# Optimization experiments

Measured on AMD Instinct MI355X. Metric: run time of the kernel, lower is better.

The kernel has to match this reference:

```python
import jax, jax.numpy as jnp
import numpy as np
import math

C_IN, L, D, H, DFF = 16, 1024, 128, 8, 512
B = 16
EPS = 1e-5


def layer_norm(x, g, b):
    mu = jnp.mean(x, axis=-1, keepdims=True)
    var = jnp.var(x, axis=-1, keepdims=True)
    return (x - mu) * jax.lax.rsqrt(var + EPS) * g + b


def tape_pe():
    pos = jnp.arange(L, dtype=jnp.float32)[:, None]
    div = jnp.exp(jnp.arange(0, D, 2, dtype=jnp.float32) * (-math.log(10000.0) / D))
    ang = pos * div * (D / L)  # [L, D/2]
    return jnp.stack([jnp.sin(ang), jnp.cos(ang)], axis=-1).reshape(L, D)


def setup_inputs() -> dict:
    key = jax.random.key(0)
    ks = jax.random.split(key, 16)
    d4 = 4 * D
    inp = {
        "x": jax.random.normal(ks[0], (B, C_IN, L), dtype=jnp.float32),
        "conv1_w": jax.random.normal(ks[1], (d4, 1, 1, 7), dtype=jnp.float32) * 0.2,
        "conv1_b": jnp.zeros((d4,), jnp.float32),
        "bn1_g": jnp.ones((d4,), jnp.float32),
        "bn1_b": jnp.zeros((d4,), jnp.float32),
        "conv2_w": jax.random.normal(ks[2], (D, d4, C_IN, 1), dtype=jnp.float32) * (1.0 / math.sqrt(d4 * C_IN)),
        "conv2_b": jnp.zeros((D,), jnp.float32),
        "bn2_g": jnp.ones((D,), jnp.float32),
        "bn2_b": jnp.zeros((D,), jnp.float32),
        "wq": jax.random.normal(ks[3], (D, D), dtype=jnp.float32) / math.sqrt(D),
        "wk": jax.random.normal(ks[4], (D, D), dtype=jnp.float32) / math.sqrt(D),
        "wv": jax.random.normal(ks[5], (D, D), dtype=jnp.float32) / math.sqrt(D),
        "rel_table": jax.random.normal(ks[6], (2 * L - 1, H), dtype=jnp.float32) * 0.02,
        "ln_att_g": jnp.ones((D,), jnp.float32),
        "ln_att_b": jnp.zeros((D,), jnp.float32),
        "ln1_g": jnp.ones((D,), jnp.float32),
        "ln1_b": jnp.zeros((D,), jnp.float32),
        "ln2_g": jnp.ones((D,), jnp.float32),
        "ln2_b": jnp.zeros((D,), jnp.float32),
        "ff_w1": jax.random.normal(ks[7], (DFF, D), dtype=jnp.float32) / math.sqrt(D),
        "ff_b1": jnp.zeros((DFF,), jnp.float32),
        "ff_w2": jax.random.normal(ks[8], (D, DFF), dtype=jnp.float32) / math.sqrt(DFF),
        "ff_b2": jnp.zeros((D,), jnp.float32),
    }
    return inp


def reference(x, conv1_w, conv1_b, bn1_g, bn1_b, conv2_w, conv2_b, bn2_g, bn2_b,
              wq, wk, wv, rel_table, ln_att_g, ln_att_b, ln1_g, ln1_b,
              ln2_g, ln2_b, ff_w1, ff_b1, ff_w2, ff_b2):
    dn = ("NCHW", "OIHW", "NCHW")
    h = x[:, None, :, :]  # [B,1,C_IN,L]
    h = jax.lax.conv_general_dilated(h, conv1_w, (1, 1), ((0, 0), (3, 3)), dimension_numbers=dn)
    h = h + conv1_b[None, :, None, None]
    # BatchNorm2d in eval with running_mean=0, running_var=1
    h = h * (bn1_g * (1.0 / math.sqrt(1.0 + EPS)))[None, :, None, None] + bn1_b[None, :, None, None]
    h = jax.nn.gelu(h, approximate=False)
    h = jax.lax.conv_general_dilated(h, conv2_w, (1, 1), ((0, 0), (0, 0)), dimension_numbers=dn)
    h = h + conv2_b[None, :, None, None]
    h = h * (bn2_g * (1.0 / math.sqrt(1.0 + EPS)))[None, :, None, None] + bn2_b[None, :, None, None]
    h = jax.nn.gelu(h, approximate=False)
    x_src = jnp.transpose(h[:, :, 0, :], (0, 2, 1))  # [B,L,D]

    x_pos = x_src + tape_pe()  # tAPE (dropout is identity in eval)

    dh = D // H
    scale = D ** (-0.5)  # note: full d_model, as in the source
    q = (x_pos @ wq.T).reshape(B, L, H, dh).transpose(0, 2, 1, 3)
    k = (x_pos @ wk.T).reshape(B, L, H, dh).transpose(0, 2, 1, 3)
    v = (x_pos @ wv.T).reshape(B, L, H, dh).transpose(0, 2, 1, 3)
    scores = jnp.einsum("bhqd,bhkd->bhqk", q, k) * scale
    attn = jax.nn.softmax(scores, axis=-1)
    # gathered relative-position bias added AFTER softmax (faithful to source)
    idx = jnp.arange(L)[:, None] - jnp.arange(L)[None, :] + (L - 1)  # [L,L]
    rel_bias = rel_table[idx]  # [L,L,H]
    attn = attn + jnp.transpose(rel_bias, (2, 0, 1))[None]
    out = jnp.einsum("bhqk,bhkd->bhqd", attn, v).transpose(0, 2, 1, 3).reshape(B, L, D)
    out = layer_norm(out, ln_att_g, ln_att_b)  # Attention_Rel_Scl.to_out

    att = layer_norm(x_src + out, ln1_g, ln1_b)
    ff = jax.nn.relu(att @ ff_w1.T + ff_b1) @ ff_w2.T + ff_b2
    y = layer_norm(att + ff, ln2_g, ln2_b)
    return jnp.transpose(y, (0, 2, 1))  # [B,D,L]
```

## Files before the change

kernel.cpp:

```cpp
#include <hip/hip_runtime.h>
#include <math.h>

#define BB   16
#define CIN  16
#define LL   1024
#define DD   128
#define NHH  8
#define DHH  16
#define DF   512

#define INVS 0.9999950000374998f
#define QSCALE 0.08838834764831845f

typedef __attribute__((ext_vector_type(4))) float f32x4;
typedef __attribute__((ext_vector_type(8))) __bf16 bf16x8;

__device__ __forceinline__ float gelu_t(float v) {
    float u = v * v;
    float a = v * fmaf(-0.07135481627f, u, -1.5957691216f);
    float e = __expf(a);
    return v * __builtin_amdgcn_rcpf(1.0f + e);
}

__device__ __forceinline__ unsigned pkbf(float a, float b) {
    union { __bf16 h[2]; unsigned u; } z;
    z.h[0] = (__bf16)a; z.h[1] = (__bf16)b;
    return z.u;
}

#define SWZ(l) ((((l) & 7) ^ (((l) >> 2) & 6)))

__global__ __launch_bounds__(256) void k_prep(
    const float* __restrict__ c2w,
    const float* __restrict__ wq, const float* __restrict__ wk,
    const float* __restrict__ wv,
    const float* __restrict__ w1f, const float* __restrict__ w2f,
    const float* __restrict__ c1w, const float* __restrict__ c1b,
    const float* __restrict__ g1,  const float* __restrict__ bb1,
    __bf16* __restrict__ w2bf,  __bf16* __restrict__ wallbf,
    __bf16* __restrict__ w1fbf, __bf16* __restrict__ w2fbf,
    float* __restrict__ peb, float* __restrict__ w1A, float* __restrict__ b1A)
{
    const int bid = blockIdx.x;
    const int t = threadIdx.x;
    if (bid < 1024) {
        int i = (bid * 256 + t) * 4;
        float4 v = *(const float4*)&c2w[i];
        union { __bf16 h[4]; float2 f2; } u;
        u.h[0] = (__bf16)v.x; u.h[1] = (__bf16)v.y;
        u.h[2] = (__bf16)v.z; u.h[3] = (__bf16)v.w;
        *(float2*)&w2bf[i] = u.f2;
    } else if (bid < 1072) {
        int e = ((bid - 1024) * 256 + t) * 4;
        int sel = e >> 14, r = e & 16383;
        const float* src = (sel == 0) ? wq : ((sel == 1) ? wk : wv);
        float sc = (sel == 0) ? QSCALE : 1.0f;
        float4 v = *(const float4*)&src[r];
        union { __bf16 h[4]; float2 f2; } u;
        u.h[0] = (__bf16)(v.x * sc); u.h[1] = (__bf16)(v.y * sc);
        u.h[2] = (__bf16)(v.z * sc); u.h[3] = (__bf16)(v.w * sc);
        *(float2*)&wallbf[e] = u.f2;
    } else if (bid < 1136) {
        int e = ((bid - 1072) * 256 + t) * 4;
        float4 v = *(const float4*)&w1f[e];
        union { __bf16 h[4]; float2 f2; } u;
        u.h[0] = (__bf16)v.x; u.h[1] = (__bf16)v.y;
        u.h[2] = (__bf16)v.z; u.h[3] = (__bf16)v.w;
        *(float2*)&w1fbf[e] = u.f2;
    } else if (bid < 1200) {
        int e = ((bid - 1136) * 256 + t) * 4;
        float4 v = *(const float4*)&w2f[e];
        union { __bf16 h[4]; float2 f2; } u;
        u.h[0] = (__bf16)v.x; u.h[1] = (__bf16)v.y;
        u.h[2] = (__bf16)v.z; u.h[3] = (__bf16)v.w;
        *(float2*)&w2fbf[e] = u.f2;
    } else if (bid < 1456) {
        int p = (bid - 1200) * 256 + t;
        int l = p >> 6, jj = p & 63;
        float ang = (float)l * expf(-0.14391156831212787f * (float)jj) * 0.125f;
        peb[l * 128 + jj * 2]     = sinf(ang);
        peb[l * 128 + jj * 2 + 1] = cosf(ang);
    } else {
        for (int o = t; o < DF; o += 256) {
            float A = g1[o] * INVS;
            #pragma unroll
            for (int tp = 0; tp < 7; tp++) w1A[o * 8 + tp] = c1w[o * 7 + tp] * A;
            w1A[o * 8 + 7] = 0.0f;
            b1A[o] = fmaf(c1b[o], A, bb1[o]);
        }
    }
}

__global__ __launch_bounds__(512, 4) void k_conv(
    const float* __restrict__ x,
    const float* __restrict__ w1A, const float* __restrict__ b1A,
    const __bf16* __restrict__ w2bf,
    const float* __restrict__ c2b, const float* __restrict__ g2,
    const float* __restrict__ bb2,
    float* __restrict__ xsrc)
{
    const int lt = blockIdx.x;
    const int b  = blockIdx.y;
    const int t  = threadIdx.x;
    const int l0 = lt * 32;

    __shared__ float xs[CIN][40];
    __shared__ __align__(16) __bf16 Ab[2][32 * 256];

    for (int idx = t; idx < CIN * 38; idx += 512) {
        int c = idx / 38, i = idx % 38;
        int l = l0 - 3 + i;
        xs[c][i] = (l >= 0 && l < LL) ? x[(b * CIN + c) * LL + l] : 0.0f;
    }
    __syncthreads();

    const int lane = t & 63;
    const int wv   = t >> 6;
    const int ogu  = __builtin_amdgcn_readfirstlane(wv);
    const int cp   = lane & 7;
    const int lqi  = lane >> 3;
    const int c0   = cp * 2;
    const int lq   = lqi * 4;

    float xw[2][10];
    #pragma unroll
    for (int j = 0; j < 10; j++) {
        xw[0][j] = xs[c0][lq + j];
        xw[1][j] = xs[c0 + 1][lq + j];
    }

    const int l15 = lane & 15, kg = lane >> 4;

    f32x4 acc[2];
    acc[0] = (f32x4){0.f, 0.f, 0.f, 0.f};
    acc[1] = (f32x4){0.f, 0.f, 0.f, 0.f};

    bf16x8 breg[8];

#define BLOAD(CH) do { \
    _Pragma("unroll") \
    for (int kk = 0; kk < 8; kk++) \
        breg[kk] = *(const bf16x8*)&w2bf[ \
            (size_t)(wv * 16 + l15) * 8192 + (size_t)(CH) * 256 + kk * 32 + kg * 8]; \
} while (0)

#define CONV_CHUNK(BUF, CH) do { \
    _Pragma("unroll") \
    for (int j = 0; j < 2; j++) { \
        int o = (CH) * 16 + ogu * 2 + j; \
        f32x4 wA = *(const f32x4*)&w1A[o * 8]; \
        f32x4 wB = *(const f32x4*)&w1A[o * 8 + 4]; \
        float bias = b1A[o]; \
        int kcol = (ogu * 2 + j) * 16 + c0; \
        _Pragma("unroll") \
        for (int dl = 0; dl < 4; dl++) { \
            float h2[2]; \
            _Pragma("unroll") \
            for (int ci = 0; ci < 2; ci++) { \
                float s = fmaf(xw[ci][dl], wA[0], bias); \
                s = fmaf(xw[ci][dl + 1], wA[1], s); \
                s = fmaf(xw[ci][dl + 2], wA[2], s); \
                s = fmaf(xw[ci][dl + 3], wA[3], s); \
                s = fmaf(xw[ci][dl + 4], wB[0], s); \
                s = fmaf(xw[ci][dl + 5], wB[1], s); \
                s = fmaf(xw[ci][dl + 6], wB[2], s); \
                h2[ci] = gelu_t(s); \
            } \
            int l = lq + dl; \
            *(unsigned*)&Ab[BUF][l * 256 + (kcol ^ (SWZ(l) << 3))] = pkbf(h2[0], h2[1]); \
        } \
    } \
} while (0)

#define MFMA_CHUNK(BUF) do { \
    _Pragma("unroll") \
    for (int kk = 0; kk < 8; kk++) { \
        int kb = kk * 32 + kg * 8; \
        _Pragma("unroll") \
        for (int mf = 0; mf < 2; mf++) { \
            int r = mf * 16 + l15; \
            bf16x8 af = *(const bf16x8*)&Ab[BUF][r * 256 + (kb ^ (SWZ(r) << 3))]; \
            acc[mf] = __builtin_amdgcn_mfma_f32_16x16x32_bf16(af, breg[kk], acc[mf], 0, 0, 0); \
        } \
    } \
} while (0)

    BLOAD(0);
    CONV_CHUNK(0, 0);
    __syncthreads();

    for (int ic = 0; ic < 30; ic += 2) {
        MFMA_CHUNK(0);
        BLOAD(ic + 1);
        CONV_CHUNK(1, ic + 1);
        __syncthreads();

        MFMA_CHUNK(1);
        BLOAD(ic + 2);
        CONV_CHUNK(0, ic + 2);
        __syncthreads();
    }
    MFMA_CHUNK(0);
    BLOAD(31);
    CONV_CHUNK(1, 31);
    __syncthreads();
    MFMA_CHUNK(1);

    {
        int d = wv * 16 + l15;
        float A2 = g2[d] * INVS;
        float B2 = fmaf(c2b[d], A2, bb2[d]);
        #pragma unroll
        for (int mf = 0; mf < 2; mf++) {
            #pragma unroll
            for (int r = 0; r < 4; r++) {
                int l = l0 + mf * 16 + kg * 4 + r;
                xsrc[((size_t)b * LL + l) * DD + d] = gelu_t(fmaf(acc[mf][r], A2, B2));
            }
        }
    }
#undef BLOAD
#undef CONV_CHUNK
#undef MFMA_CHUNK
}

__global__ __launch_bounds__(384) void k_qkv(
    const float* __restrict__ xsrc, const float* __restrict__ peb,
    const __bf16* __restrict__ wallbf,
    __bf16* __restrict__ qo, __bf16* __restrict__ ko, __bf16* __restrict__ vo)
{
    const int lt = blockIdx.x, b = blockIdx.y;
    const int t = threadIdx.x;
    const int l0 = lt * 64;

    __shared__ __align__(16) __bf16 Xp[64 * 128];

    for (int e = t; e < 2048; e += 384) {
        int l = e >> 5, d0 = (e & 31) * 4;
        float4 xv = *(const float4*)&xsrc[((size_t)b * LL + l0 + l) * DD + d0];
        float4 pv = *(const float4*)&peb[(size_t)(l0 + l) * DD + d0];
        union { __bf16 h[4]; float2 f2; } u;
        u.h[0] = (__bf16)(xv.x + pv.x); u.h[1] = (__bf16)(xv.y + pv.y);
        u.h[2] = (__bf16)(xv.z + pv.z); u.h[3] = (__bf16)(xv.w + pv.w);
        *(float2*)&Xp[l * 128 + (d0 ^ (SWZ(l) << 3))] = u.f2;
    }
    __syncthreads();

    const int w = t >> 6, lane = t & 63;
    const int l15 = lane & 15, kg = lane >> 4;
    const int wsel = w >> 1, hb = w & 1;

    bf16x8 breg[16];
    #pragma unroll
    for (int nf = 0; nf < 4; nf++)
        #pragma unroll
        for (int kk = 0; kk < 4; kk++)
            breg[nf * 4 + kk] = *(const bf16x8*)&wallbf[
                (size_t)wsel * 16384 + (size_t)(hb * 64 + nf * 16 + l15) * 128 + kk * 32 + kg * 8];

    f32x4 acc[4][4];
    #pragma unroll
    for (int mf = 0; mf < 4; mf++)
        #pragma unroll
        for (int nf = 0; nf < 4; nf++) acc[mf][nf] = (f32x4){0.f, 0.f, 0.f, 0.f};

    #pragma unroll
    for (int kk = 0; kk < 4; kk++) {
        int kb = kk * 32 + kg * 8;
        bf16x8 af[4];
        #pragma unroll
        for (int mf = 0; mf < 4; mf++) {
            int r = mf * 16 + l15;
            af[mf] = *(const bf16x8*)&Xp[r * 128 + (kb ^ (SWZ(r) << 3))];
        }
        #pragma unroll
        for (int mf = 0; mf < 4; mf++)
            #pragma unroll
            for (int nf = 0; nf < 4; nf++)
                acc[mf][nf] = __builtin_amdgcn_mfma_f32_16x16x32_bf16(
                    af[mf], breg[nf * 4 + kk], acc[mf][nf], 0, 0, 0);
    }

    __bf16* op = (wsel == 0) ? qo : ((wsel == 1) ? ko : vo);
    #pragma unroll
    for (int mf = 0; mf < 4; mf++) {
        #pragma unroll
        for (int nf = 0; nf < 4; nf++) {
            int h = hb * 4 + nf;
            #pragma unroll
            for (int r = 0; r < 4; r++) {
                int l = l0 + mf * 16 + kg * 4 + r;
                op[(((size_t)b * NHH + h) * LL + l) * DHH + l15] = (__bf16)acc[mf][nf][r];
            }
        }
    }
}

__global__ __launch_bounds__(256) void k_attn(
    const __bf16* __restrict__ q, const __bf16* __restrict__ k,
    const __bf16* __restrict__ v, const float* __restrict__ rel,
    float* __restrict__ out)
{
    const int bh = blockIdx.x;
    const int qt = blockIdx.y;
    const int h  = bh & 7;
    const int t  = threadIdx.x;
    const int w  = t >> 6, lane = t & 63;
    const int g  = lane >> 4, qi = lane & 15;
    const int xq = (qi & 7) << 3;
    const int qbase = qt * 128 + w * 32;

    __shared__ __align__(16) __bf16 lds[16384];
    __bf16* Vl = lds;
    __bf16* Pw = lds + 4096 + w * 2048;
    __bf16* R0 = lds + 12288;
    __bf16* R1 = lds + 14336;

    for (int i = t; i < 2048; i += 256) {
        R0[i] = (__bf16)((i <= 2046) ? rel[(size_t)(2046 - i) * NHH + h] : 0.0f);
        R1[i] = (__bf16)((i <= 2045) ? rel[(size_t)(2045 - i) * NHH + h] : 0.0f);
    }

    bf16x8 qf[2];
    {
        union { unsigned u[4]; bf16x8 v8; } uz;
        uz.u[0] = uz.u[1] = uz.u[2] = uz.u[3] = 0u;
        #pragma unroll
        for (int n = 0; n < 2; n++) {
            qf[n] = uz.v8;
            if (g < 2)
                qf[n] = *(const bf16x8*)&q[((size_t)bh * LL + qbase + n * 16 + qi) * DHH + g * 8];
        }
    }

    f32x4 accp[2], accb[2];
    #pragma unroll
    for (int n = 0; n < 2; n++) {
        accp[n] = (f32x4){0.f, 0.f, 0.f, 0.f};
        accb[n] = (f32x4){0.f, 0.f, 0.f, 0.f};
    }
    float mrun[2] = {-INFINITY, -INFINITY};
    float lrun[2] = {0.f, 0.f};

    const f32x4 zero4 = (f32x4){0.f, 0.f, 0.f, 0.f};

#define PROC_N(Sn, n) do { \
    float mx = Sn[0][0]; \
    _Pragma("unroll") \
    for (int f = 0; f < 8; f++) { \
        _Pragma("unroll") \
        for (int r = 0; r < 4; r++) if (f || r) mx = fmaxf(mx, Sn[f][r]); } \
    mx = fmaxf(mx, __shfl_xor(mx, 16, 64)); \
    mx = fmaxf(mx, __shfl_xor(mx, 32, 64)); \
    float mnew = fmaxf(mrun[n], mx); \
    float sf = __expf(mrun[n] - mnew); \
    mrun[n] = mnew; \
    lrun[n] *= sf; \
    accp[n][0] *= sf; accp[n][1] *= sf; accp[n][2] *= sf; accp[n][3] *= sf; \
    float ls = 0.f; \
    _Pragma("unroll") \
    for (int f = 0; f < 8; f++) { \
        float p0 = __expf(Sn[f][0] - mnew), p1 = __expf(Sn[f][1] - mnew); \
        float p2 = __expf(Sn[f][2] - mnew), p3 = __expf(Sn[f][3] - mnew); \
        ls += (p0 + p1) + (p2 + p3); \
        unsigned* pp = (unsigned*)(Pw + (qi * 128 + ((f * 16 + g * 4) ^ xq))); \
        pp[0] = pkbf(p0, p1); pp[1] = pkbf(p2, p3); \
    } \
    ls += __shfl_xor(ls, 16, 64); ls += __shfl_xor(ls, 32, 64); \
    lrun[n] += ls; \
    int qoff = 1023 - (qbase + (n) * 16 + qi) + k0; \
    _Pragma("unroll") \
    for (int c = 0; c < 4; c++) { \
        bf16x8 vf = *(const bf16x8*)&Vbuf[qi * 128 + ((c * 32 + g * 8) ^ xq)]; \
        bf16x8 pf = *(const bf16x8*)&Pw[qi * 128 + ((c * 32 + g * 8) ^ xq)]; \
        int idx = qoff + c * 32 + 8 * g; \
        const unsigned* tb = (const unsigned*)((idx & 1) ? R1 : R0); \
        unsigned s_ = (unsigned)idx >> 1; \
        union { unsigned u[4]; bf16x8 v8; } bu; \
        bu.u[0] = tb[s_]; bu.u[1] = tb[s_ + 1]; \
        bu.u[2] = tb[s_ + 2]; bu.u[3] = tb[s_ + 3]; \
        accp[n] = __builtin_amdgcn_mfma_f32_16x16x32_bf16(vf, pf, accp[n], 0, 0, 0); \
        accb[n] = __builtin_amdgcn_mfma_f32_16x16x32_bf16(vf, bu.v8, accb[n], 0, 0, 0); \
    } \
} while (0)

    for (int kt = 0; kt < 8; kt++) {
        const int k0 = kt * 128;
        {
            int kr = t >> 1, d0 = (t & 1) * 8;
            bf16x8 b8 = *(const bf16x8*)&v[((size_t)bh * LL + k0 + kr) * DHH + d0];
            __bf16* dst = Vl + (kt & 1) * 2048;
            #pragma unroll
            for (int i = 0; i < 8; i++) {
                int d = d0 + i;
                dst[d * 128 + (kr ^ ((d & 7) << 3))] = b8[i];
            }
        }
        __syncthreads();
        const __bf16* Vbuf = Vl + (kt & 1) * 2048;

        f32x4 S0[8], S1[8];
        #pragma unroll
        for (int f = 0; f < 8; f++) {
            bf16x8 kf = *(const bf16x8*)&k[((size_t)bh * LL + k0 + f * 16 + qi) * DHH + (g & 1) * 8];
            S0[f] = __builtin_amdgcn_mfma_f32_16x16x32_bf16(kf, qf[0], zero4, 0, 0, 0);
            S1[f] = __builtin_amdgcn_mfma_f32_16x16x32_bf16(kf, qf[1], zero4, 0, 0, 0);
        }

        PROC_N(S0, 0);
        PROC_N(S1, 1);
    }
#undef PROC_N

    #pragma unroll
    for (int n = 0; n < 2; n++) {
        float inv = 1.0f / lrun[n];
        float4 o;
        o.x = accp[n][0] * inv + accb[n][0];
        o.y = accp[n][1] * inv + accb[n][1];
        o.z = accp[n][2] * inv + accb[n][2];
        o.w = accp[n][3] * inv + accb[n][3];
        *(float4*)&out[((size_t)bh * LL + qbase + n * 16 + qi) * DHH + g * 4] = o;
    }
}

__global__ __launch_bounds__(256) void k_ln(
    const float* __restrict__ ao,  const float* __restrict__ xsrc,
    const float* __restrict__ lag, const float* __restrict__ lab,
    const float* __restrict__ l1g, const float* __restrict__ l1b,
    float* __restrict__ att)
{
    const int lt = blockIdx.x, b = blockIdx.y;
    const int t = threadIdx.x;
    const int l0 = lt * 64;
    __shared__ float tile[64][132];

    #pragma unroll
    for (int u = 0; u < 4; u++) {
        int cid = u * 256 + t;
        int hh = cid >> 7, rem = cid & 127;
        int l = rem >> 1, dh0 = (rem & 1) * 8;
        const float* src = &ao[(((size_t)b * NHH + hh) * LL + l0 + l) * DHH + dh0];
        float4 a0 = *(const float4*)src;
        float4 a1 = *(const float4*)(src + 4);
        *(float4*)&tile[l][hh * 16 + dh0]     = a0;
        *(float4*)&tile[l][hh * 16 + dh0 + 4] = a1;
    }
    __syncthreads();

    const int wid = t >> 6, lane = t & 63;
    float2 ga  = *(const float2*)&lag[lane * 2];
    float2 ba  = *(const float2*)&lab[lane * 2];
    float2 g1v = *(const float2*)&l1g[lane * 2];
    float2 b1v = *(const float2*)&l1b[lane * 2];

    for (int rr = 0; rr < 16; rr++) {
        int r = wid * 16 + rr;
        float2 vv = *(const float2*)&tile[r][lane * 2];
        float s = vv.x + vv.y, s2 = vv.x * vv.x + vv.y * vv.y;
        #pragma unroll
        for (int m = 1; m < 64; m <<= 1) { s += __shfl_xor(s, m, 64); s2 += __shfl_xor(s2, m, 64); }
        float mu = s * (1.f / 128.f);
        float var = s2 * (1.f / 128.f) - mu * mu;
        float rs = rsqrtf(var + 1e-5f);
        float o0 = (vv.x - mu) * rs * ga.x + ba.x;
        float o1 = (vv.y - mu) * rs * ga.y + ba.y;
        float2 xv = *(const float2*)&xsrc[((size_t)b * LL + l0 + r) * DD + lane * 2];
        float t0 = xv.x + o0, t1 = xv.y + o1;
        s = t0 + t1; s2 = t0 * t0 + t1 * t1;
        #pragma unroll
        for (int m = 1; m < 64; m <<= 1) { s += __shfl_xor(s, m, 64); s2 += __shfl_xor(s2, m, 64); }
        mu = s * (1.f / 128.f);
        var = s2 * (1.f / 128.f) - mu * mu;
        rs = rsqrtf(var + 1e-5f);
        float a0 = (t0 - mu) * rs * g1v.x + b1v.x;
        float a1 = (t1 - mu) * rs * g1v.y + b1v.y;
        float2 o = {a0, a1};
        *(float2*)&att[((size_t)b * LL + l0 + r) * DD + lane * 2] = o;
    }
}

__global__ __launch_bounds__(512) void k_ff1(
    const float* __restrict__ att, const __bf16* __restrict__ w1fbf,
    const float* __restrict__ b1f, __bf16* __restrict__ ff1b)
{
    const int lt = blockIdx.x, b = blockIdx.y;
    const int t = threadIdx.x;
    const int l0 = lt * 64;

    __shared__ __align__(16) __bf16 Ax[64 * 128];

    #pragma unroll
    for (int it = 0; it < 4; it++) {
        int e = it * 512 + t;
        int l = e >> 5, d0 = (e & 31) * 4;
        float4 xv = *(const float4*)&att[((size_t)b * LL + l0 + l) * DD + d0];
        union { __bf16 h[4]; float2 f2; } u;
        u.h[0] = (__bf16)xv.x; u.h[1] = (__bf16)xv.y;
        u.h[2] = (__bf16)xv.z; u.h[3] = (__bf16)xv.w;
        *(float2*)&Ax[l * 128 + (d0 ^ (SWZ(l) << 3))] = u.f2;
    }
    __syncthreads();

    const int w = t >> 6, lane = t & 63;
    const int l15 = lane & 15, kg = lane >> 4;

    bf16x8 breg[16];
    #pragma unroll
    for (int nf = 0; nf < 4; nf++)
        #pragma unroll
        for (int kk = 0; kk < 4; kk++)
            breg[nf * 4 + kk] = *(const bf16x8*)&w1fbf[
                (size_t)(w * 64 + nf * 16 + l15) * 128 + kk * 32 + kg * 8];

    f32x4 acc[4][4];
    #pragma unroll
    for (int mf = 0; mf < 4; mf++)
        #pragma unroll
        for (int nf = 0; nf < 4; nf++) acc[mf][nf] = (f32x4){0.f, 0.f, 0.f, 0.f};

    #pragma unroll
    for (int kk = 0; kk < 4; kk++) {
        int kb = kk * 32 + kg * 8;
        bf16x8 af[4];
        #pragma unroll
        for (int mf = 0; mf < 4; mf++) {
            int r = mf * 16 + l15;
            af[mf] = *(const bf16x8*)&Ax[r * 128 + (kb ^ (SWZ(r) << 3))];
        }
        #pragma unroll
        for (int mf = 0; mf < 4; mf++)
            #pragma unroll
            for (int nf = 0; nf < 4; nf++)
                acc[mf][nf] = __builtin_amdgcn_mfma_f32_16x16x32_bf16(
                    af[mf], breg[nf * 4 + kk], acc[mf][nf], 0, 0, 0);
    }

    #pragma unroll
    for (int nf = 0; nf < 4; nf++) {
        int n = w * 64 + nf * 16 + l15;
        float bias = b1f[n];
        #pragma unroll
        for (int mf = 0; mf < 4; mf++) {
            #pragma unroll
            for (int r = 0; r < 4; r++) {
                int l = l0 + mf * 16 + kg * 4 + r;
                float vv = fmaxf(acc[mf][nf][r] + bias, 0.0f);
                ff1b[((size_t)b * LL + l) * DF + n] = (__bf16)vv;
            }
        }
    }
}

__global__ __launch_bounds__(512) void k_ff2(
    const __bf16* __restrict__ ff1b, const __bf16* __restrict__ w2fbf,
    const float* __restrict__ b2f, const float* __restrict__ att,
    const float* __restrict__ l2g, const float* __restrict__ l2b,
    float* __restrict__ y)
{
    const int lt = blockIdx.x, b = blockIdx.y;
    const int t = threadIdx.x;
    const int l0 = lt * 64;

    __shared__ __align__(16) __bf16 Ax[64 * 512];
    float* yl = (float*)Ax;

    #pragma unroll
    for (int it = 0; it < 8; it++) {
        int g8 = it * 512 + t;
        int l = g8 >> 6, c8 = g8 & 63;
        bf16x8 v8 = *(const bf16x8*)&ff1b[((size_t)b * LL + l0 + l) * DF + c8 * 8];
        *(bf16x8*)&Ax[l * 512 + ((c8 * 8) ^ (SWZ(l) << 3))] = v8;
    }
    __syncthreads();

    const int w = t >> 6, lane = t & 63;
    const int l15 = lane & 15, kg = lane >> 4;
    const int d = w * 16 + l15;

    bf16x8 breg[16];
    #pragma unroll
    for (int kk = 0; kk < 16; kk++)
        breg[kk] = *(const bf16x8*)&w2fbf[(size_t)d * DF + kk * 32 + kg * 8];

    f32x4 acc[4];
    #pragma unroll
    for (int mf = 0; mf < 4; mf++) acc[mf] = (f32x4){0.f, 0.f, 0.f, 0.f};

    #pragma unroll
    for (int kk = 0; kk < 16; kk++) {
        int kb = kk * 32 + kg * 8;
        #pragma unroll
        for (int mf = 0; mf < 4; mf++) {
            int r = mf * 16 + l15;
            bf16x8 af = *(const bf16x8*)&Ax[r * 512 + (kb ^ (SWZ(r) << 3))];
            acc[mf] = __builtin_amdgcn_mfma_f32_16x16x32_bf16(af, breg[kk], acc[mf], 0, 0, 0);
        }
    }
    __syncthreads();

    {
        float bias = b2f[d];
        #pragma unroll
        for (int mf = 0; mf < 4; mf++) {
            #pragma unroll
            for (int r = 0; r < 4; r++) {
                int l = mf * 16 + kg * 4 + r;
                float res = att[((size_t)b * LL + l0 + l) * DD + d];
                yl[l * 132 + d] = acc[mf][r] + bias + res;
            }
        }
    }
    __syncthreads();

    const int wid = t >> 6;
    float2 gv = *(const float2*)&l2g[lane * 2];
    float2 bv = *(const float2*)&l2b[lane * 2];
    for (int rr = 0; rr < 8; rr++) {
        int r = wid * 8 + rr;
        float2 vv = *(const float2*)&yl[r * 132 + lane * 2];
        float s = vv.x + vv.y, s2 = vv.x * vv.x + vv.y * vv.y;
        #pragma unroll
        for (int m = 1; m < 64; m <<= 1) { s += __shfl_xor(s, m, 64); s2 += __shfl_xor(s2, m, 64); }
        float mu = s * (1.f / 128.f);
        float var = s2 * (1.f / 128.f) - mu * mu;
        float rs = rsqrtf(var + 1e-5f);
        float o0 = (vv.x - mu) * rs * gv.x + bv.x;
        float o1 = (vv.y - mu) * rs * gv.y + bv.y;
        yl[r * 132 + lane * 2]     = o0;
        yl[r * 132 + lane * 2 + 1] = o1;
    }
    __syncthreads();

    {
        int dd = t >> 2, lh = (t & 3) * 16;
        #pragma unroll
        for (int i0 = 0; i0 < 16; i0 += 4) {
            float4 o = { yl[(lh + i0 + 0) * 132 + dd], yl[(lh + i0 + 1) * 132 + dd],
                         yl[(lh + i0 + 2) * 132 + dd], yl[(lh + i0 + 3) * 132 + dd] };
            *(float4*)&y[(size_t)b * DD * LL + (size_t)dd * LL + l0 + lh + i0] = o;
        }
    }
}

extern "C" void kernel_launch(void* const* d_in, const int* in_sizes, int n_in,
                              void* d_out, int out_size, void* d_ws, size_t ws_size,
                              hipStream_t stream)
{
    const float* x   = (const float*)d_in[0];
    const float* c1w = (const float*)d_in[1];
    const float* c1b = (const float*)d_in[2];
    const float* g1  = (const float*)d_in[3];
    const float* bb1 = (const float*)d_in[4];
    const float* c2w = (const float*)d_in[5];
    const float* c2b = (const float*)d_in[6];
    const float* g2  = (const float*)d_in[7];
    const float* bb2 = (const float*)d_in[8];
    const float* wq  = (const float*)d_in[9];
    const float* wk  = (const float*)d_in[10];
    const float* wv  = (const float*)d_in[11];
    const float* rel = (const float*)d_in[12];
    const float* lag = (const float*)d_in[13];
    const float* lab = (const float*)d_in[14];
    const float* l1g = (const float*)d_in[15];
    const float* l1b = (const float*)d_in[16];
    const float* l2g = (const float*)d_in[17];
    const float* l2b = (const float*)d_in[18];
    const float* w1f = (const float*)d_in[19];
    const float* b1f = (const float*)d_in[20];
    const float* w2f = (const float*)d_in[21];
    const float* b2f = (const float*)d_in[22];

    char* W = (char*)d_ws;
    const size_t MB = 1ull << 20;
    float*  xsrc   = (float*)(W);
    float*  abuf   = (float*)(W + 8 * MB);
    float*  attb   = (float*)(W + 16 * MB);
    __bf16* qbuf   = (__bf16*)(W + 24 * MB);
    __bf16* kbuf   = (__bf16*)(W + 28 * MB);
    __bf16* vbuf   = (__bf16*)(W + 32 * MB);
    __bf16* ff1b   = (__bf16*)(W + 36 * MB);
    __bf16* w2bf   = (__bf16*)(W + 52 * MB);
    __bf16* wallbf = (__bf16*)(W + 54 * MB);
    __bf16* w1fbf  = (__bf16*)(W + 54 * MB + 128 * 1024);
    __bf16* w2fbf  = (__bf16*)(W + 54 * MB + 256 * 1024);
    float*  peb    = (float*)(W + 54 * MB + 384 * 1024);
    float*  w1A    = (float*)(W + 54 * MB + 896 * 1024);
    float*  b1A    = (float*)(W + 54 * MB + 912 * 1024);

    k_prep<<<dim3(1457), dim3(256), 0, stream>>>(
        c2w, wq, wk, wv, w1f, w2f, c1w, c1b, g1, bb1,
        w2bf, wallbf, w1fbf, w2fbf, peb, w1A, b1A);
    k_conv<<<dim3(32, 16), dim3(512), 0, stream>>>(x, w1A, b1A, w2bf, c2b, g2, bb2, xsrc);
    k_qkv<<<dim3(16, 16), dim3(384), 0, stream>>>(xsrc, peb, wallbf, qbuf, kbuf, vbuf);
    k_attn<<<dim3(128, 8), dim3(256), 0, stream>>>(qbuf, kbuf, vbuf, rel, abuf);
    k_ln<<<dim3(16, 16), dim3(256), 0, stream>>>(abuf, xsrc, lag, lab, l1g, l1b, attb);
    k_ff1<<<dim3(16, 16), dim3(512), 0, stream>>>(attb, w1fbf, b1f, ff1b);
    k_ff2<<<dim3(16, 16), dim3(512), 0, stream>>>(ff1b, w2fbf, b2f, attb, l2g, l2b, (float*)d_out);
}
```

Before: 240.7 us.

## Retile conv2 waves as 2x4 grid, pack conv1 FMAs and use exp2 GELU

The fused conv kernel's waves are rearranged from eight column strips, each covering all 32 rows, into a 2x4 grid where each wave owns 16 rows by 32 output channels. Each wave now reads half as many shared-memory A fragments but loads twice as many conv2 weight vectors, so total global weight traffic per block doubles. The depthwise conv1 accumulation is rewritten on float2 vectors so the compiler can emit packed FMAs for the two input channels. The tanh-style GELU folds log2(e) into its constants and calls the native exp2 builtin instead of __expf.

New measurement: 350.2 us. +45.5%, slower.

```diff
diff --git a/kernel.cpp b/kernel.cpp
--- a/kernel.cpp
+++ b/kernel.cpp
@@ -12,14 +12,27 @@
 #define INVS 0.9999950000374998f
 #define QSCALE 0.08838834764831845f
 
+typedef __attribute__((ext_vector_type(2))) float f32x2;
 typedef __attribute__((ext_vector_type(4))) float f32x4;
 typedef __attribute__((ext_vector_type(8))) __bf16 bf16x8;
 
 __device__ __forceinline__ float gelu_t(float v) {
     float u = v * v;
-    float a = v * fmaf(-0.07135481627f, u, -1.5957691216f);
-    float e = __expf(a);
+    float a = v * fmaf(-0.10294425f, u, -2.3022082f);
+    float e = __builtin_amdgcn_exp2f(a);
     return v * __builtin_amdgcn_rcpf(1.0f + e);
+}
+
+__device__ __forceinline__ f32x2 gelu2(f32x2 v) {
+    f32x2 u = v * v;
+    f32x2 a = v * (u * (-0.10294425f) + (-2.3022082f));
+    f32x2 e;
+    e.x = __builtin_amdgcn_exp2f(a.x);
+    e.y = __builtin_amdgcn_exp2f(a.y);
+    f32x2 r;
+    r.x = __builtin_amdgcn_rcpf(1.0f + e.x);
+    r.y = __builtin_amdgcn_rcpf(1.0f + e.y);
+    return v * r;
 }
 
 __device__ __forceinline__ unsigned pkbf(float a, float b) {
@@ -115,19 +128,18 @@
     __syncthreads();
 
     const int lane = t & 63;
-    const int wv   = t >> 6;
-    const int ogu  = __builtin_amdgcn_readfirstlane(wv);
+    const int ogu  = __builtin_amdgcn_readfirstlane(t >> 6);
+    const int mw   = ogu >> 2;
+    const int nw   = ogu & 3;
     const int cp   = lane & 7;
     const int lqi  = lane >> 3;
     const int c0   = cp * 2;
     const int lq   = lqi * 4;
 
-    float xw[2][10];
-    #pragma unroll
-    for (int j = 0; j < 10; j++) {
-        xw[0][j] = xs[c0][lq + j];
-        xw[1][j] = xs[c0 + 1][lq + j];
-    }
+    f32x2 xw2[10];
+    #pragma unroll
+    for (int j = 0; j < 10; j++)
+        xw2[j] = (f32x2){xs[c0][lq + j], xs[c0 + 1][lq + j]};
 
     const int l15 = lane & 15, kg = lane >> 4;
 
@@ -135,13 +147,15 @@
     acc[0] = (f32x4){0.f, 0.f, 0.f, 0.f};
     acc[1] = (f32x4){0.f, 0.f, 0.f, 0.f};
 
-    bf16x8 breg[8];
+    bf16x8 breg[16];
 
 #define BLOAD(CH) do { \
     _Pragma("unroll") \
-    for (int kk = 0; kk < 8; kk++) \
-        breg[kk] = *(const bf16x8*)&w2bf[ \
-            (size_t)(wv * 16 + l15) * 8192 + (size_t)(CH) * 256 + kk * 32 + kg * 8]; \
+    for (int nf = 0; nf < 2; nf++) \
+        _Pragma("unroll") \
+        for (int kk = 0; kk < 8; kk++) \
+            breg[nf * 8 + kk] = *(const bf16x8*)&w2bf[ \
+                (size_t)(nw * 32 + nf * 16 + l15) * 8192 + (size_t)(CH) * 256 + kk * 32 + kg * 8]; \
 } while (0)
 
 #define CONV_CHUNK(BUF, CH) do { \
@@ -154,20 +168,17 @@
         int kcol = (ogu * 2 + j) * 16 + c0; \
         _Pragma("unroll") \
         for (int dl = 0; dl < 4; dl++) { \
-            float h2[2]; \
-            _Pragma("unroll") \
-            for (int ci = 0; ci < 2; ci++) { \
-                float s = fmaf(xw[ci][dl], wA[0], bias); \
-                s = fmaf(xw[ci][dl + 1], wA[1], s); \
-                s = fmaf(xw[ci][dl + 2], wA[2], s); \
-                s = fmaf(xw[ci][dl + 3], wA[3], s); \
-                s = fmaf(xw[ci][dl + 4], wB[0], s); \
-                s = fmaf(xw[ci][dl + 5], wB[1], s); \
-                s = fmaf(xw[ci][dl + 6], wB[2], s); \
-                h2[ci] = gelu_t(s); \
-            } \
+            f32x2 s = (f32x2){bias, bias}; \
+            s = s + xw2[dl]     * wA[0]; \
+            s = s + xw2[dl + 1] * wA[1]; \
+            s = s + xw2[dl + 2] * wA[2]; \
+            s = s + xw2[dl + 3] * wA[3]; \
+            s = s + xw2[dl + 4] * wB[0]; \
+            s = s + xw2[dl + 5] * wB[1]; \
+            s = s + xw2[dl + 6] * wB[2]; \
+            f32x2 g = gelu2(s); \
             int l = lq + dl; \
-            *(unsigned*)&Ab[BUF][l * 256 + (kcol ^ (SWZ(l) << 3))] = pkbf(h2[0], h2[1]); \
+            *(unsigned*)&Ab[BUF][l * 256 + (kcol ^ (SWZ(l) << 3))] = pkbf(g.x, g.y); \
         } \
     } \
 } while (0)
@@ -176,12 +187,10 @@
     _Pragma("unroll") \
     for (int kk = 0; kk < 8; kk++) { \
         int kb = kk * 32 + kg * 8; \
-        _Pragma("unroll") \
-        for (int mf = 0; mf < 2; mf++) { \
-            int r = mf * 16 + l15; \
-            bf16x8 af = *(const bf16x8*)&Ab[BUF][r * 256 + (kb ^ (SWZ(r) << 3))]; \
-            acc[mf] = __builtin_amdgcn_mfma_f32_16x16x32_bf16(af, breg[kk], acc[mf], 0, 0, 0); \
-        } \
+        int r_ = mw * 16 + l15; \
+        bf16x8 af = *(const bf16x8*)&Ab[BUF][r_ * 256 + (kb ^ (SWZ(r_) << 3))]; \
+        acc[0] = __builtin_amdgcn_mfma_f32_16x16x32_bf16(af, breg[kk],     acc[0], 0, 0, 0); \
+        acc[1] = __builtin_amdgcn_mfma_f32_16x16x32_bf16(af, breg[8 + kk], acc[1], 0, 0, 0); \
     } \
 } while (0)
 
@@ -206,17 +215,15 @@
     __syncthreads();
     MFMA_CHUNK(1);
 
-    {
-        int d = wv * 16 + l15;
+    #pragma unroll
+    for (int nf = 0; nf < 2; nf++) {
+        int d = nw * 32 + nf * 16 + l15;
         float A2 = g2[d] * INVS;
         float B2 = fmaf(c2b[d], A2, bb2[d]);
         #pragma unroll
-        for (int mf = 0; mf < 2; mf++) {
-            #pragma unroll
-            for (int r = 0; r < 4; r++) {
-                int l = l0 + mf * 16 + kg * 4 + r;
-                xsrc[((size_t)b * LL + l) * DD + d] = gelu_t(fmaf(acc[mf][r], A2, B2));
-            }
+        for (int r = 0; r < 4; r++) {
+            int l = l0 + mw * 16 + kg * 4 + r;
+            xsrc[((size_t)b * LL + l) * DD + d] = gelu_t(fmaf(acc[nf][r], A2, B2));
         }
     }
 #undef BLOAD
```
